# Optimization experiments

Hardware: AMD Instinct MI355X
Metric: run time of the kernel (lower is better)

Reference implementation:

```python
import jax, jax.numpy as jnp
import numpy as np

D_MODEL, D_INNER, D_STATE, NHEADS, HEADDIM, D_CONV, CHUNK = 1024, 2048, 128, 32, 64, 4, 64
B_SZ, L = 2, 2048
EPS = 1e-5


def _segsum_exp(x):
    # x: (..., T) -> exp of lower-triangular cumulative segment sums, (..., T, T)
    cs = jnp.cumsum(x, axis=-1)
    seg = cs[..., :, None] - cs[..., None, :]
    T = x.shape[-1]
    mask = jnp.tril(jnp.ones((T, T), dtype=bool))
    return jnp.exp(jnp.where(mask, seg, 0.0)) * mask


def ssd(x, A, B, C, chunk):
    # x: (b,l,h,p), A: (b,l,h), B,C: (b,l,n)
    b, l, h, p = x.shape
    n = B.shape[-1]
    c = l // chunk
    x = x.reshape(b, c, chunk, h, p)
    A = A.reshape(b, c, chunk, h).transpose(0, 3, 1, 2)        # (b,h,c,s)
    B = B.reshape(b, c, chunk, n)
    C = C.reshape(b, c, chunk, n)
    A_cum = jnp.cumsum(A, axis=-1)                              # (b,h,c,s)
    Lmat = _segsum_exp(A)                                       # (b,h,c,s,s)
    # intra-chunk (diagonal block) output
    Y_diag = jnp.einsum('bcln,bcsn,bhcls,bcshp->bclhp', C, B, Lmat, x)
    # per-chunk final states
    decay_states = jnp.exp(A_cum[..., -1:] - A_cum)             # (b,h,c,s)
    states = jnp.einsum('bcsn,bhcs,bcshp->bchpn', B, decay_states, x)
    states = jnp.concatenate([jnp.zeros_like(states[:, :1]), states], axis=1)  # (b,c+1,h,p,n)
    # inter-chunk recurrence over chunk sums
    chunk_sums = jnp.pad(A_cum[..., -1], ((0, 0), (0, 0), (1, 0)))  # (b,h,c+1)
    decay_chunk = _segsum_exp(chunk_sums)                       # (b,h,c+1,c+1)
    new_states = jnp.einsum('bhzc,bchpn->bzhpn', decay_chunk, states)
    states_in, final_state = new_states[:, :-1], new_states[:, -1]
    out_decay = jnp.exp(A_cum)                                  # (b,h,c,s)
    Y_off = jnp.einsum('bcln,bchpn,bhcl->bclhp', C, states_in, out_decay)
    Y = (Y_diag + Y_off).reshape(b, l, h, p)
    return Y, final_state


def causal_depthwise_conv(x, w, b):
    # x: (B, C, L), w: (C, K), b: (C,)
    K = w.shape[-1]
    Llen = x.shape[-1]
    xp = jnp.pad(x, ((0, 0), (0, 0), (K - 1, 0)))
    out = b[None, :, None]
    for k in range(K):
        out = out + w[None, :, k, None] * xp[:, :, k:k + Llen]
    return out


def setup_inputs() -> dict:
    key = jax.random.key(0)
    ks = jax.random.split(key, 9)
    d_in_proj = 2 * D_INNER + 2 * D_STATE + NHEADS
    conv_dim = D_INNER + 2 * D_STATE
    return {
        'u': jax.random.normal(ks[0], (B_SZ, L, D_MODEL), jnp.float32),
        'W_in': jax.random.normal(ks[1], (d_in_proj, D_MODEL), jnp.float32) * (D_MODEL ** -0.5),
        'conv_w': jax.random.normal(ks[2], (conv_dim, D_CONV), jnp.float32) * (D_CONV ** -0.5),
        'conv_b': jax.random.normal(ks[3], (conv_dim,), jnp.float32) * 0.01,
        'dt_bias': jax.random.normal(ks[4], (NHEADS,), jnp.float32),
        'A_log': jnp.log(1.0 + 15.0 * jax.random.uniform(ks[5], (NHEADS,), jnp.float32)),
        'D': jax.random.normal(ks[6], (NHEADS,), jnp.float32),
        'norm_w': jnp.ones((D_INNER,), jnp.float32),
        'W_out': jax.random.normal(ks[8], (D_MODEL, D_INNER), jnp.float32) * (D_INNER ** -0.5),
    }


def reference(u, W_in, conv_w, conv_b, dt_bias, A_log, D, norm_w, W_out):
    zxbcdt = u @ W_in.T                                        # (B,L,d_in_proj)
    z = zxbcdt[..., :D_INNER]
    xBC = zxbcdt[..., D_INNER:2 * D_INNER + 2 * D_STATE]
    dt = jax.nn.softplus(zxbcdt[..., -NHEADS:] + dt_bias)      # (B,L,H)
    # causal depthwise conv + silu
    xBC = causal_depthwise_conv(xBC.transpose(0, 2, 1), conv_w, conv_b).transpose(0, 2, 1)
    xBC = jax.nn.silu(xBC)
    A = -jnp.exp(A_log)                                        # (H,)
    x = xBC[..., :D_INNER].reshape(u.shape[0], u.shape[1], NHEADS, HEADDIM)
    Bm = xBC[..., D_INNER:D_INNER + D_STATE]
    Cm = xBC[..., D_INNER + D_STATE:]
    y, _ = ssd(x * dt[..., None], A * dt, Bm, Cm, CHUNK)
    y = y + x * D[:, None]
    y = y.reshape(u.shape[0], u.shape[1], D_INNER)
    # gated RMSNorm
    y = y * jax.nn.silu(z)
    y = y * jax.lax.rsqrt(jnp.mean(y * y, axis=-1, keepdims=True) + EPS) * norm_w
    return y @ W_out.T
```

## Files before the change

kernel.cpp:

```cpp
#include <hip/hip_runtime.h>
#include <hip/hip_bf16.h>
#include <math.h>

#define D_MODEL 1024
#define D_INNER 2048
#define D_STATE 128
#define NHEADS 32
#define HEADDIM 64
#define CHUNK 64
#define B_SZ 2
#define LSEQ 2048
#define BL (B_SZ*LSEQ)
#define DPROJ (2*D_INNER + 2*D_STATE + NHEADS)
#define CONV_DIM (D_INNER + 2*D_STATE)
#define NCHUNK (LSEQ/CHUNK)
#define NPAD1 4480
#define EPSF 1e-5f

typedef __attribute__((ext_vector_type(8))) _Float16 half8;
typedef __attribute__((ext_vector_type(4))) _Float16 half4;
typedef __attribute__((ext_vector_type(4))) float f32x4;

__device__ __forceinline__ float siluf(float v){ return v / (1.0f + expf(-v)); }
__device__ __forceinline__ float softplusf(float v){ return v > 20.0f ? v : log1pf(expf(v)); }
__device__ __forceinline__ unsigned short f2h(float x){
  union { _Float16 h; unsigned short u; } v; v.h = (_Float16)x;
  return v.u;
}
__device__ __forceinline__ float h2f(unsigned short x){
  union { unsigned short u; _Float16 h; } v; v.u = x;
  return (float)v.h;
}
__device__ __forceinline__ _Float16 h2h(unsigned short x){
  union { unsigned short u; _Float16 h; } v; v.u = x;
  return v.h;
}

typedef const __attribute__((address_space(1))) void gvoid_t;
typedef __attribute__((address_space(3))) void lvoid_t;
__device__ __forceinline__ void gl_lds16(const void* gsrc, void* ldst) {
  gvoid_t* g = reinterpret_cast<gvoid_t*>((uintptr_t)gsrc);
  lvoid_t* l = reinterpret_cast<lvoid_t*>((unsigned int)(uintptr_t)ldst);
  __builtin_amdgcn_global_load_lds(g, l, 16, 0, 0);
}

__global__ void cvt_f16(const float* __restrict__ in, unsigned short* __restrict__ out, int n4) {
  int i = blockIdx.x*256 + threadIdx.x;
  if (i >= n4) return;
  float4 v = *(const float4*)(in + (size_t)i*4);
  ushort4 o; o.x=f2h(v.x); o.y=f2h(v.y); o.z=f2h(v.z); o.w=f2h(v.w);
  *(ushort4*)(out + (size_t)i*4) = o;
}

__global__ void cvt_pad(const float* __restrict__ in, unsigned short* __restrict__ out,
                        int rows_in, int total4, int kdim4) {
  int i = blockIdx.x*256 + threadIdx.x;
  if (i >= total4) return;
  int row = i / kdim4;
  ushort4 o; o.x=0; o.y=0; o.z=0; o.w=0;
  if (row < rows_in) {
    float4 v = *(const float4*)(in + (size_t)i*4);
    o.x=f2h(v.x); o.y=f2h(v.y); o.z=f2h(v.z); o.w=f2h(v.w);
  }
  *(ushort4*)(out + (size_t)i*4) = o;
}

template<int OUT_F16>
__global__ __launch_bounds__(256) void gemm_f16_pipe(const unsigned short* __restrict__ A,
    const unsigned short* __restrict__ W, void* __restrict__ Cv, int N, int K) {
  __shared__ unsigned short lds[5*2*4096];
  const int t   = threadIdx.x;
  const int wid = t >> 6, l = t & 63;
  const int nwg = gridDim.x * gridDim.y;
  int bid = blockIdx.y * gridDim.x + blockIdx.x;
  int swz = (bid & 7) * (nwg >> 3) + (bid >> 3);
  const int m0 = (swz / gridDim.x) * 128;
  const int n0 = (swz % gridDim.x) * 128;
  const int wr = wid >> 1, wc = wid & 1;
  const int fr = l & 15, cg = l >> 4;
  const int NT = K >> 5;

  int srow[2]; int scol[2];
  #pragma unroll
  for (int i=0;i<2;++i){
    int s = i*256 + t;
    int r = s >> 2, c = s & 3;
    int sw = (r + (r>>2)) & 3;
    srow[i] = r; scol[i] = (c ^ sw) * 8;
  }
  const unsigned short* Abase = A + (size_t)m0 * K;
  const unsigned short* Wbase = W + (size_t)n0 * K;

#define STAGE(tt, slot) { \
    int kk = (tt) << 5; \
    unsigned short* La = &lds[(slot)*8192]; \
    unsigned short* Lb = &lds[(slot)*8192 + 4096]; \
    gl_lds16(Abase + (size_t)srow[0]*K + kk + scol[0], (char*)La + (0*256+t)*16); \
    gl_lds16(Abase + (size_t)srow[1]*K + kk + scol[1], (char*)La + (1*256+t)*16); \
    gl_lds16(Wbase + (size_t)srow[0]*K + kk + scol[0], (char*)Lb + (0*256+t)*16); \
    gl_lds16(Wbase + (size_t)srow[1]*K + kk + scol[1], (char*)Lb + (1*256+t)*16); \
  }

  f32x4 acc[4][4] = {};
  STAGE(0, 0);
  STAGE(1, 1);
  STAGE(2, 2);
  STAGE(3, 3);
  asm volatile("s_waitcnt vmcnt(12)" ::: "memory");
  __builtin_amdgcn_s_barrier();
  asm volatile("" ::: "memory");

  int cs = 0;
  for (int tt = 0; tt < NT; ++tt) {
    int ss = (cs == 0) ? 4 : cs - 1;
    if (tt + 4 < NT) STAGE(tt+4, ss);
    const unsigned short* La = &lds[cs*8192];
    const unsigned short* Lb = &lds[cs*8192 + 4096];
    half8 af[4], bfv[4];
    #pragma unroll
    for (int m=0;m<4;++m){
      int r = wr*64 + m*16 + fr;
      int sw = (r + (r>>2)) & 3;
      af[m] = *(const half8*)&La[(r*4 + (cg ^ sw))*8];
    }
    #pragma unroll
    for (int n=0;n<4;++n){
      int r = wc*64 + n*16 + fr;
      int sw = (r + (r>>2)) & 3;
      bfv[n] = *(const half8*)&Lb[(r*4 + (cg ^ sw))*8];
    }
    __builtin_amdgcn_s_setprio(1);
    #pragma unroll
    for (int m=0;m<4;++m)
      #pragma unroll
      for (int n=0;n<4;++n)
        acc[m][n] = __builtin_amdgcn_mfma_f32_16x16x32_f16(af[m], bfv[n], acc[m][n], 0, 0, 0);
    __builtin_amdgcn_s_setprio(0);
    if (tt + 1 < NT) {
      if      (tt + 4 < NT) { asm volatile("s_waitcnt vmcnt(12)" ::: "memory"); }
      else if (tt + 3 < NT) { asm volatile("s_waitcnt vmcnt(8)"  ::: "memory"); }
      else if (tt + 2 < NT) { asm volatile("s_waitcnt vmcnt(4)"  ::: "memory"); }
      else                  { asm volatile("s_waitcnt vmcnt(0)"  ::: "memory"); }
      __builtin_amdgcn_s_barrier();
      asm volatile("" ::: "memory");
    }
    cs = (cs == 4) ? 0 : cs + 1;
  }
#undef STAGE

  const int crow = m0 + wr*64 + (l >> 4) * 4;
  const int ccol0 = n0 + wc*64 + fr;
  #pragma unroll
  for (int m = 0; m < 4; ++m) {
    #pragma unroll
    for (int n = 0; n < 4; ++n) {
      int col = ccol0 + n*16;
      if (col < N) {
        if (OUT_F16) {
          unsigned short* cp = (unsigned short*)Cv + (size_t)(crow + m*16)*N + col;
          #pragma unroll
          for (int j = 0; j < 4; ++j) cp[(size_t)j*N] = f2h(acc[m][n][j]);
        } else {
          float* cp = (float*)Cv + (size_t)(crow + m*16)*N + col;
          #pragma unroll
          for (int j = 0; j < 4; ++j) cp[(size_t)j*N] = acc[m][n][j];
        }
      }
    }
  }
}

__global__ void dtx_kernel(const unsigned short* __restrict__ zx,
    const float* __restrict__ dt_bias, float* __restrict__ dt) {
  int i = blockIdx.x*256 + threadIdx.x;
  if (i >= BL*NHEADS) return;
  int row = i >> 5, h = i & 31;
  float v = h2f(zx[(size_t)row*DPROJ + (2*D_INNER + 2*D_STATE) + h]) + dt_bias[h];
  dt[i] = softplusf(v);
}

__global__ __launch_bounds__(64) void acum_kernel(const float* __restrict__ dt,
    const float* __restrict__ A_log, float* __restrict__ A_cum) {
  int blk = blockIdx.x;
  int c = blk & 31, h = (blk >> 5) & 31, b = blk >> 10;
  int l = threadIdx.x;
  __shared__ float sv[64];
  int row = b*LSEQ + c*CHUNK + l;
  float a = -expf(A_log[h]);
  sv[l] = a * dt[row*NHEADS + h];
  __syncthreads();
  if (l == 0) {
    float s = 0.f;
    for (int i=0;i<64;++i){ s += sv[i]; sv[i] = s; }
  }
  __syncthreads();
  A_cum[blk*64 + l] = sv[l];
}

__global__ __launch_bounds__(256) void conv8_kernel(const unsigned short* __restrict__ zx,
    const float* __restrict__ w, const float* __restrict__ bias, unsigned short* __restrict__ xBC) {
  int idx = blockIdx.x*256 + threadIdx.x;
  if (idx >= (BL/8)*(CONV_DIM/4)) return;
  int c4  = idx % (CONV_DIM/4);
  int rb  = idx / (CONV_DIM/4);
  int ch  = c4 * 4;
  int row0 = rb * 8;
  int l0   = row0 & (LSEQ-1);
  float4 r[11];
  #pragma unroll
  for (int jj=0;jj<11;++jj){
    int li = l0 + jj - 3;
    if (li >= 0) {
      ushort4 v = *(const ushort4*)&zx[(size_t)(row0 + jj - 3)*DPROJ + D_INNER + ch];
      r[jj] = make_float4(h2f(v.x), h2f(v.y), h2f(v.z), h2f(v.w));
    } else r[jj] = make_float4(0.f,0.f,0.f,0.f);
  }
  float4 wv[4];
  #pragma unroll
  for (int c=0;c<4;++c) wv[c] = *(const float4*)&w[(ch+c)*4];
  float4 bv = *(const float4*)&bias[ch];
  #pragma unroll
  for (int j=0;j<8;++j){
    float4 acc = bv;
    acc.x += wv[0].x*r[j].x + wv[0].y*r[j+1].x + wv[0].z*r[j+2].x + wv[0].w*r[j+3].x;
    acc.y += wv[1].x*r[j].y + wv[1].y*r[j+1].y + wv[1].z*r[j+2].y + wv[1].w*r[j+3].y;
    acc.z += wv[2].x*r[j].z + wv[2].y*r[j+1].z + wv[2].z*r[j+2].z + wv[2].w*r[j+3].z;
    acc.w += wv[3].x*r[j].w + wv[3].y*r[j+1].w + wv[3].z*r[j+2].w + wv[3].w*r[j+3].w;
    ushort4 o; o.x=f2h(siluf(acc.x)); o.y=f2h(siluf(acc.y)); o.z=f2h(siluf(acc.z)); o.w=f2h(siluf(acc.w));
    *(ushort4*)&xBC[(size_t)(row0+j)*CONV_DIM + ch] = o;
  }
}

__global__ __launch_bounds__(256) void g_kernel(const unsigned short* __restrict__ xBC, float* __restrict__ G) {
  int blk = blockIdx.x >> 2;
  int lq  = blockIdx.x & 3;
  int b = blk >> 5, c = blk & 31;
  __shared__ float Bsh[64][129];
  int t = threadIdx.x;
  int row0 = b*LSEQ + c*CHUNK;
  for (int j=0;j<32;++j){
    int lin = j*256 + t;
    int s = lin >> 7, n = lin & 127;
    Bsh[s][n] = h2f(xBC[(size_t)(row0+s)*CONV_DIM + D_INNER + n]);
  }
  __syncthreads();
  int l = lq*16 + (t >> 4), s0 = (t & 15) * 4;
  const unsigned short* Cp = &xBC[(size_t)(row0+l)*CONV_DIM + D_INNER + D_STATE];
  float acc[4] = {};
  for (int n=0;n<128;++n){
    float cv = h2f(Cp[n]);
    #pragma unroll
    for (int j=0;j<4;++j) acc[j] += cv * Bsh[s0+j][n];
  }
  float* Gp = &G[(size_t)blk*4096 + l*64 + s0];
  #pragma unroll
  for (int j=0;j<4;++j) Gp[j] = acc[j];
}

__global__ __launch_bounds__(256) void states_mfma(const unsigned short* __restrict__ xBC,
    const float* __restrict__ dt, const float* __restrict__ A_cum, unsigned short* __restrict__ states) {
  int blk = blockIdx.x;
  int h = blk & 31, c = (blk>>5)&31, b = blk>>10;
  __shared__ _Float16 Bt[128][72];
  __shared__ _Float16 xdT[64][72];
  __shared__ float Ac[64], dtl[64];
  int t = threadIdx.x;
  int wid = t >> 6, ln = t & 63;
  int row0 = b*LSEQ + c*CHUNK;
  if (t < 64){ Ac[t] = A_cum[((b*32+h)*32 + c)*64 + t]; dtl[t] = dt[(row0+t)*NHEADS + h]; }
  __syncthreads();
  float AcL = Ac[63];
  #pragma unroll
  for (int j=0;j<32;++j){
    int lin = j*256+t; int s = lin>>7, n = lin&127;
    Bt[n][s] = h2h(xBC[(size_t)(row0+s)*CONV_DIM + D_INNER + n]);
  }
  #pragma unroll
  for (int j=0;j<16;++j){
    int lin = j*256+t; int s = lin>>6, p = lin&63;
    xdT[p][s] = (_Float16)(h2f(xBC[(size_t)(row0+s)*CONV_DIM + h*HEADDIM + p]) * dtl[s] * expf(AcL - Ac[s]));
  }
  __syncthreads();
  const int fr = ln & 15, fk = (ln >> 4) * 8;
  f32x4 acc[4][2] = {};
  #pragma unroll
  for (int ks = 0; ks < 2; ++ks){
    half8 a[4], bb[2];
    #pragma unroll
    for (int pt=0;pt<4;++pt) a[pt] = *(const half8*)&xdT[pt*16+fr][ks*32+fk];
    #pragma unroll
    for (int nt=0;nt<2;++nt) bb[nt] = *(const half8*)&Bt[(wid*2+nt)*16+fr][ks*32+fk];
    #pragma unroll
    for (int pt=0;pt<4;++pt)
      #pragma unroll
      for (int nt=0;nt<2;++nt)
        acc[pt][nt] = __builtin_amdgcn_mfma_f32_16x16x32_f16(a[pt], bb[nt], acc[pt][nt], 0, 0, 0);
  }
  unsigned short* Sp = &states[(size_t)blk*8192];
  #pragma unroll
  for (int pt=0;pt<4;++pt){
    int p0 = pt*16 + (ln>>4)*4;
    #pragma unroll
    for (int nt=0;nt<2;++nt){
      int n = (wid*2+nt)*16 + fr;
      #pragma unroll
      for (int j=0;j<4;++j) Sp[(p0+j)*128 + n] = f2h(acc[pt][nt][j]);
    }
  }
}

__global__ __launch_bounds__(256) void scan_kernel(const float* __restrict__ A_cum,
                                                   unsigned short* __restrict__ states) {
  int g  = blockIdx.x & 7;
  int bh = blockIdx.x >> 3;
  int b = bh >> 5, h = bh & 31;
  int t = threadIdx.x;
  float S[4];
  #pragma unroll
  for (int j=0;j<4;++j) S[j] = 0.f;
  for (int c=0;c<NCHUNK;++c){
    float decay = expf(A_cum[((b*32+h)*32 + c)*64 + 63]);
    unsigned short* Sp = &states[(size_t)((b*32+c)*32 + h)*8192];
    #pragma unroll
    for (int j=0;j<4;++j){
      float tmp = h2f(Sp[(g*4+j)*256+t]);
      Sp[(g*4+j)*256+t] = f2h(S[j]);
      S[j] = S[j]*decay + tmp;
    }
  }
}

__global__ __launch_bounds__(256) void y_mfma(const unsigned short* __restrict__ xBC,
    const unsigned short* __restrict__ zx, const float* __restrict__ dt,
    const float* __restrict__ A_cum, const float* __restrict__ G,
    const unsigned short* __restrict__ states, const float* __restrict__ Dp,
    unsigned short* __restrict__ y_pre) {
  int blk = blockIdx.x;
  int h = blk & 31, c = (blk>>5)&31, b = blk>>10;
  __shared__ _Float16 Cl[64][136];
  __shared__ _Float16 Sin[64][136];
  __shared__ _Float16 Ms[64][72];
  __shared__ _Float16 xdT[64][72];
  __shared__ float Ac[64], dtl[64];
  int t = threadIdx.x;
  int wid = t >> 6, ln = t & 63;
  int row0 = b*LSEQ + c*CHUNK;
  if (t < 64){ Ac[t] = A_cum[((b*32+h)*32 + c)*64 + t]; dtl[t] = dt[(row0+t)*NHEADS + h]; }
  __syncthreads();
  #pragma unroll
  for (int j=0;j<32;++j){
    int lin = j*256+t; int l = lin>>7, n = lin&127;
    Cl[l][n] = (_Float16)(h2f(xBC[(size_t)(row0+l)*CONV_DIM + D_INNER + D_STATE + n]) * expf(Ac[l]));
  }
  {
    const unsigned short* Sg = &states[(size_t)blk*8192];
    #pragma unroll
    for (int j=0;j<8;++j){
      int elem = (j*256+t)*4; int p = elem>>7, n = elem&127;
      ushort4 v = *(const ushort4*)&Sg[elem];
      half4 hv = { h2h(v.x), h2h(v.y), h2h(v.z), h2h(v.w) };
      *(half4*)&Sin[p][n] = hv;
    }
  }
  #pragma unroll
  for (int j=0;j<16;++j){
    int lin = j*256+t; int s = lin>>6, p = lin&63;
    xdT[p][s] = (_Float16)(h2f(xBC[(size_t)(row0+s)*CONV_DIM + h*HEADDIM + p]) * dtl[s]);
  }
  {
    const float* Gp = &G[(size_t)(b*32+c)*4096];
    #pragma unroll
    for (int j=0;j<16;++j){
      int lin = j*256+t; int l = lin>>6, s = lin&63;
      Ms[l][s] = (s <= l) ? (_Float16)(Gp[l*64+s] * expf(Ac[l]-Ac[s])) : (_Float16)0.f;
    }
  }
  __syncthreads();
  const int wr = wid >> 1, wc = wid & 1;
  const int fr = ln & 15, fk = (ln >> 4) * 8;
  f32x4 acc[2][2] = {};
  #pragma unroll
  for (int ks = 0; ks < 4; ++ks){
    half8 a[2], bb[2];
    #pragma unroll
    for (int lt=0;lt<2;++lt) a[lt] = *(const half8*)&Cl[(wr*2+lt)*16+fr][ks*32+fk];
    #pragma unroll
    for (int pt=0;pt<2;++pt) bb[pt] = *(const half8*)&Sin[(wc*2+pt)*16+fr][ks*32+fk];
    #pragma unroll
    for (int lt=0;lt<2;++lt)
      #pragma unroll
      for (int pt=0;pt<2;++pt)
        acc[lt][pt] = __builtin_amdgcn_mfma_f32_16x16x32_f16(a[lt], bb[pt], acc[lt][pt], 0, 0, 0);
  }
  #pragma unroll
  for (int ks = 0; ks < 2; ++ks){
    half8 a[2], bb[2];
    #pragma unroll
    for (int lt=0;lt<2;++lt) a[lt] = *(const half8*)&Ms[(wr*2+lt)*16+fr][ks*32+fk];
    #pragma unroll
    for (int pt=0;pt<2;++pt) bb[pt] = *(const half8*)&xdT[(wc*2+pt)*16+fr][ks*32+fk];
    #pragma unroll
    for (int lt=0;lt<2;++lt)
      #pragma unroll
      for (int pt=0;pt<2;++pt)
        acc[lt][pt] = __builtin_amdgcn_mfma_f32_16x16x32_f16(a[lt], bb[pt], acc[lt][pt], 0, 0, 0);
  }
  float Dh = Dp[h];
  #pragma unroll
  for (int lt=0;lt<2;++lt){
    int l0 = (wr*2+lt)*16 + (ln>>4)*4;
    #pragma unroll
    for (int pt=0;pt<2;++pt){
      int p = (wc*2+pt)*16 + fr;
      #pragma unroll
      for (int j=0;j<4;++j){
        int grow = row0 + l0 + j;
        float x = h2f(xBC[(size_t)grow*CONV_DIM + h*HEADDIM + p]);
        float z = h2f(zx[(size_t)grow*DPROJ + h*HEADDIM + p]);
        y_pre[(size_t)grow*D_INNER + h*HEADDIM + p] = f2h((acc[lt][pt][j] + x*Dh) * siluf(z));
      }
    }
  }
}

__global__ __launch_bounds__(256) void rms_kernel(const unsigned short* __restrict__ y,
    const float* __restrict__ norm_w, unsigned short* __restrict__ yh) {
  int row = blockIdx.x;
  int t = threadIdx.x;
  const unsigned short* yr = y + (size_t)row*D_INNER + t*8;
  ushort4 a = *(const ushort4*)yr;
  ushort4 bq = *(const ushort4*)(yr+4);
  float v[8];
  v[0]=h2f(a.x); v[1]=h2f(a.y); v[2]=h2f(a.z); v[3]=h2f(a.w);
  v[4]=h2f(bq.x); v[5]=h2f(bq.y); v[6]=h2f(bq.z); v[7]=h2f(bq.w);
  float ss = 0.f;
  #pragma unroll
  for (int j=0;j<8;++j) ss += v[j]*v[j];
  #pragma unroll
  for (int off=32; off>0; off>>=1) ss += __shfl_down(ss, off, 64);
  __shared__ float wsum[4];
  int wid = t >> 6, lane = t & 63;
  if (lane == 0) wsum[wid] = ss;
  __syncthreads();
  if (t == 0) wsum[0] = rsqrtf((wsum[0]+wsum[1]+wsum[2]+wsum[3])/D_INNER + EPSF);
  __syncthreads();
  float sc = wsum[0];
  float4 w0 = *(const float4*)&norm_w[t*8];
  float4 w1 = *(const float4*)&norm_w[t*8+4];
  ushort4 o0, o1;
  o0.x=f2h(v[0]*sc*w0.x); o0.y=f2h(v[1]*sc*w0.y); o0.z=f2h(v[2]*sc*w0.z); o0.w=f2h(v[3]*sc*w0.w);
  o1.x=f2h(v[4]*sc*w1.x); o1.y=f2h(v[5]*sc*w1.y); o1.z=f2h(v[6]*sc*w1.z); o1.w=f2h(v[7]*sc*w1.w);
  unsigned short* yo = yh + (size_t)row*D_INNER + t*8;
  *(ushort4*)yo = o0;
  *(ushort4*)(yo+4) = o1;
}

extern "C" void kernel_launch(void* const* d_in, const int* in_sizes, int n_in,
                              void* d_out, int out_size, void* d_ws, size_t ws_size,
                              hipStream_t stream) {
  const float* u       = (const float*)d_in[0];
  const float* W_in    = (const float*)d_in[1];
  const float* conv_w  = (const float*)d_in[2];
  const float* conv_b  = (const float*)d_in[3];
  const float* dt_bias = (const float*)d_in[4];
  const float* A_log   = (const float*)d_in[5];
  const float* Dp      = (const float*)d_in[6];
  const float* norm_w  = (const float*)d_in[7];
  const float* W_out   = (const float*)d_in[8];
  float* out = (float*)d_out;

  char* w = (char*)d_ws;
  unsigned short* zx_h   = (unsigned short*)w;  w += (size_t)BL*DPROJ*2;
  unsigned short* xBC_h  = (unsigned short*)w;  w += (size_t)BL*CONV_DIM*2;
  unsigned short* ypre_h = (unsigned short*)w;  w += (size_t)BL*D_INNER*2;
  unsigned short* y_h    = (unsigned short*)w;  w += (size_t)BL*D_INNER*2;
  unsigned short* u_h    = (unsigned short*)w;  w += (size_t)BL*D_MODEL*2;
  unsigned short* Win_h  = (unsigned short*)w;  w += (size_t)NPAD1*D_MODEL*2;
  unsigned short* Wout_h = (unsigned short*)w;  w += (size_t)D_MODEL*D_INNER*2;
  unsigned short* states = (unsigned short*)w;  w += (size_t)B_SZ*NCHUNK*NHEADS*HEADDIM*D_STATE*2;
  float* dt     = (float*)w;  w += (size_t)BL*NHEADS*4;
  float* A_cum  = (float*)w;  w += (size_t)B_SZ*NHEADS*NCHUNK*CHUNK*4;
  float* G      = (float*)w;  w += (size_t)B_SZ*NCHUNK*CHUNK*CHUNK*4;

  cvt_f16<<<(BL*D_MODEL/4)/256, 256, 0, stream>>>(u, u_h, BL*D_MODEL/4);
  cvt_pad<<<((NPAD1*D_MODEL/4)+255)/256, 256, 0, stream>>>(W_in, Win_h, DPROJ, NPAD1*D_MODEL/4, D_MODEL/4);
  cvt_f16<<<(D_MODEL*D_INNER/4)/256, 256, 0, stream>>>(W_out, Wout_h, D_MODEL*D_INNER/4);
  gemm_f16_pipe<1><<<dim3(NPAD1/128, BL/128), 256, 0, stream>>>(u_h, Win_h, zx_h, DPROJ, D_MODEL);
  dtx_kernel<<<(BL*NHEADS+255)/256, 256, 0, stream>>>(zx_h, dt_bias, dt);
  acum_kernel<<<B_SZ*NHEADS*NCHUNK, 64, 0, stream>>>(dt, A_log, A_cum);
  conv8_kernel<<<((BL/8)*(CONV_DIM/4)+255)/256, 256, 0, stream>>>(zx_h, conv_w, conv_b, xBC_h);
  g_kernel<<<B_SZ*NCHUNK*4, 256, 0, stream>>>(xBC_h, G);
  states_mfma<<<B_SZ*NCHUNK*NHEADS, 256, 0, stream>>>(xBC_h, dt, A_cum, states);
  scan_kernel<<<B_SZ*NHEADS*8, 256, 0, stream>>>(A_cum, states);
  y_mfma<<<B_SZ*NCHUNK*NHEADS, 256, 0, stream>>>(xBC_h, zx_h, dt, A_cum, G, states, Dp, ypre_h);
  rms_kernel<<<BL, 256, 0, stream>>>(ypre_h, norm_w, y_h);
  gemm_f16_pipe<0><<<dim3(D_MODEL/128, BL/128), 256, 0, stream>>>(y_h, Wout_h, out, D_MODEL, D_INNER);
}
```

Baseline: 210.7 us.

## Add 256x256-tile 512-thread GEMM for input projection

```diff
diff --git a/kernel.cpp b/kernel.cpp
--- a/kernel.cpp
+++ b/kernel.cpp
@@ -14,7 +14,7 @@
 #define DPROJ (2*D_INNER + 2*D_STATE + NHEADS)
 #define CONV_DIM (D_INNER + 2*D_STATE)
 #define NCHUNK (LSEQ/CHUNK)
-#define NPAD1 4480
+#define NPAD 4608
 #define EPSF 1e-5f
 
 typedef __attribute__((ext_vector_type(8))) _Float16 half8;
@@ -63,6 +63,106 @@
     o.x=f2h(v.x); o.y=f2h(v.y); o.z=f2h(v.z); o.w=f2h(v.w);
   }
   *(ushort4*)(out + (size_t)i*4) = o;
+}
+
+template<int OUT_F16>
+__global__ __launch_bounds__(512, 2) void gemm_f16_256(const unsigned short* __restrict__ A,
+    const unsigned short* __restrict__ W, void* __restrict__ Cv, int N, int K) {
+  __shared__ unsigned short lds[2*32768];
+  const int t   = threadIdx.x;
+  const int wid = t >> 6, l = t & 63;
+  const int nwg = gridDim.x * gridDim.y;
+  int bid = blockIdx.y * gridDim.x + blockIdx.x;
+  int swz = (bid & 7) * (nwg >> 3) + (bid >> 3);
+  const int m0 = (swz / gridDim.x) * 256;
+  const int n0 = (swz % gridDim.x) * 256;
+  const int wm = wid >> 2, wn = wid & 3;
+  const int fr = l & 15, cg = l >> 4;
+  const int NT = K >> 6;
+
+  int srow[4], scol[4];
+  #pragma unroll
+  for (int i=0;i<4;++i){
+    int c = i*512 + t;
+    int r = c >> 3, s = c & 7;
+    srow[i] = r; scol[i] = (s ^ (r & 7)) * 8;
+  }
+
+#define STG256(tile, buf) { \
+    int kk = (tile) << 6; \
+    char* La_ = (char*)lds + (buf)*65536; \
+    char* Lb_ = La_ + 32768; \
+    gl_lds16(A + (size_t)(m0+srow[0])*K + kk + scol[0], La_ + (0*512+t)*16); \
+    gl_lds16(A + (size_t)(m0+srow[1])*K + kk + scol[1], La_ + (1*512+t)*16); \
+    gl_lds16(A + (size_t)(m0+srow[2])*K + kk + scol[2], La_ + (2*512+t)*16); \
+    gl_lds16(A + (size_t)(m0+srow[3])*K + kk + scol[3], La_ + (3*512+t)*16); \
+    gl_lds16(W + (size_t)(n0+srow[0])*K + kk + scol[0], Lb_ + (0*512+t)*16); \
+    gl_lds16(W + (size_t)(n0+srow[1])*K + kk + scol[1], Lb_ + (1*512+t)*16); \
+    gl_lds16(W + (size_t)(n0+srow[2])*K + kk + scol[2], Lb_ + (2*512+t)*16); \
+    gl_lds16(W + (size_t)(n0+srow[3])*K + kk + scol[3], Lb_ + (3*512+t)*16); \
+  }
+
+  f32x4 acc[8][4] = {};
+  STG256(0, 0);
+  for (int tt = 0; tt < NT; ++tt) {
+    int buf = tt & 1;
+    if (tt + 1 < NT) {
+      STG256(tt+1, buf^1);
+      asm volatile("s_waitcnt vmcnt(8)" ::: "memory");
+    } else {
+      asm volatile("s_waitcnt vmcnt(0)" ::: "memory");
+    }
+    __builtin_amdgcn_s_barrier();
+    asm volatile("" ::: "memory");
+    const char* La = (const char*)lds + buf*65536;
+    const char* Lb = La + 32768;
+    #pragma unroll
+    for (int ks = 0; ks < 2; ++ks) {
+      half8 bfv[4];
+      #pragma unroll
+      for (int n=0;n<4;++n){
+        int r = wn*64 + n*16 + fr;
+        int kc = (ks*4 + cg) ^ (r & 7);
+        bfv[n] = *(const half8*)(Lb + r*128 + kc*16);
+      }
+      __builtin_amdgcn_s_setprio(1);
+      #pragma unroll
+      for (int m=0;m<8;++m){
+        int r = wm*128 + m*16 + fr;
+        int kc = (ks*4 + cg) ^ (r & 7);
+        half8 af = *(const half8*)(La + r*128 + kc*16);
+        #pragma unroll
+        for (int n=0;n<4;++n)
+          acc[m][n] = __builtin_amdgcn_mfma_f32_16x16x32_f16(af, bfv[n], acc[m][n], 0, 0, 0);
+      }
+      __builtin_amdgcn_s_setprio(0);
+    }
+    asm volatile("s_waitcnt lgkmcnt(0)" ::: "memory");
+    __builtin_amdgcn_s_barrier();
+    asm volatile("" ::: "memory");
+  }
+#undef STG256
+
+  const int crow0 = m0 + wm*128 + cg*4;
+  const int ccol0 = n0 + wn*64 + fr;
+  #pragma unroll
+  for (int m=0;m<8;++m){
+    #pragma unroll
+    for (int n=0;n<4;++n){
+      int col = ccol0 + n*16;
+      if (col < N) {
+        if (OUT_F16) {
+          unsigned short* cp = (unsigned short*)Cv + (size_t)(crow0 + m*16)*N + col;
+          #pragma unroll
+          for (int j=0;j<4;++j) cp[(size_t)j*N] = f2h(acc[m][n][j]);
+        } else {
+          float* cp = (float*)Cv + (size_t)(crow0 + m*16)*N + col;
+          #pragma unroll
+          for (int j=0;j<4;++j) cp[(size_t)j*N] = acc[m][n][j];
+        }
+      }
+    }
+  }
 }
 
 template<int OUT_F16>
@@ -475,7 +575,7 @@
   unsigned short* ypre_h = (unsigned short*)w;  w += (size_t)BL*D_INNER*2;
   unsigned short* y_h    = (unsigned short*)w;  w += (size_t)BL*D_INNER*2;
   unsigned short* u_h    = (unsigned short*)w;  w += (size_t)BL*D_MODEL*2;
-  unsigned short* Win_h  = (unsigned short*)w;  w += (size_t)NPAD1*D_MODEL*2;
+  unsigned short* Win_h  = (unsigned short*)w;  w += (size_t)NPAD*D_MODEL*2;
   unsigned short* Wout_h = (unsigned short*)w;  w += (size_t)D_MODEL*D_INNER*2;
   unsigned short* states = (unsigned short*)w;  w += (size_t)B_SZ*NCHUNK*NHEADS*HEADDIM*D_STATE*2;
   float* dt     = (float*)w;  w += (size_t)BL*NHEADS*4;
@@ -483,9 +583,9 @@
   float* G      = (float*)w;  w += (size_t)B_SZ*NCHUNK*CHUNK*CHUNK*4;
 
   cvt_f16<<<(BL*D_MODEL/4)/256, 256, 0, stream>>>(u, u_h, BL*D_MODEL/4);
-  cvt_pad<<<((NPAD1*D_MODEL/4)+255)/256, 256, 0, stream>>>(W_in, Win_h, DPROJ, NPAD1*D_MODEL/4, D_MODEL/4);
+  cvt_pad<<<((NPAD*D_MODEL/4)+255)/256, 256, 0, stream>>>(W_in, Win_h, DPROJ, NPAD*D_MODEL/4, D_MODEL/4);
   cvt_f16<<<(D_MODEL*D_INNER/4)/256, 256, 0, stream>>>(W_out, Wout_h, D_MODEL*D_INNER/4);
-  gemm_f16_pipe<1><<<dim3(NPAD1/128, BL/128), 256, 0, stream>>>(u_h, Win_h, zx_h, DPROJ, D_MODEL);
+  gemm_f16_256<1><<<dim3(NPAD/256, BL/256), 512, 0, stream>>>(u_h, Win_h, zx_h, DPROJ, D_MODEL);
   dtx_kernel<<<(BL*NHEADS+255)/256, 256, 0, stream>>>(zx_h, dt_bias, dt);
   acum_kernel<<<B_SZ*NHEADS*NCHUNK, 64, 0, stream>>>(dt, A_log, A_cum);
   conv8_kernel<<<((BL/8)*(CONV_DIM/4)+255)/256, 256, 0, stream>>>(zx_h, conv_w, conv_b, xBC_h);
```

Result: slower. 215.3 us (+2.2%).
